# Kernel optimization log

Hardware: AMD Instinct MI355X
Metric: run time of the kernel (lower is better)

The kernel has to match this reference:

```python
import jax, jax.numpy as jnp
import numpy as np

DIM = 1024
WIN = 7
HEADS = 16
HEAD_DIM = DIM // HEADS
NT = WIN * WIN  # tokens per window = 49


def _relative_position_index():
    coords = np.stack(np.meshgrid(np.arange(WIN), np.arange(WIN), indexing='ij'))  # [2,W,W]
    cf = coords.reshape(2, -1)  # [2, NT]
    rel = cf[:, :, None] - cf[:, None, :]  # [2, NT, NT]
    rel = rel.transpose(1, 2, 0).copy()
    rel[:, :, 0] += WIN - 1
    rel[:, :, 1] += WIN - 1
    rel[:, :, 0] *= 2 * WIN - 1
    return jnp.asarray(rel.sum(-1), dtype=jnp.int32)  # [NT, NT]

REL_IDX = _relative_position_index()


def setup_inputs() -> dict:
    key = jax.random.key(0)
    ks = jax.random.split(key, 7)
    bsz_windows = 2048
    num_windows = 64
    x = jax.random.normal(ks[0], (bsz_windows, NT, DIM), dtype=jnp.float32)
    attn_mask = jax.random.normal(ks[1], (num_windows, NT, NT), dtype=jnp.float32)
    s = 0.02
    qkv_w = jax.random.normal(ks[2], (3 * DIM, DIM), dtype=jnp.float32) * s
    qkv_b = jnp.zeros((3 * DIM,), dtype=jnp.float32)
    proj_w = jax.random.normal(ks[3], (DIM, DIM), dtype=jnp.float32) * s
    proj_b = jnp.zeros((DIM,), dtype=jnp.float32)
    bias_table = jax.random.normal(ks[4], ((2 * WIN - 1) ** 2, HEADS), dtype=jnp.float32) * s
    return {"x": x, "attn_mask": attn_mask, "qkv_w": qkv_w, "qkv_b": qkv_b,
            "proj_w": proj_w, "proj_b": proj_b, "bias_table": bias_table}


def reference(x, attn_mask, qkv_w, qkv_b, proj_w, proj_b, bias_table):
    bw, nt, c = x.shape
    scale = HEAD_DIM ** -0.5
    qkv = x @ qkv_w.T + qkv_b  # [bw, nt, 3*dim]
    qkv = qkv.reshape(bw, nt, 3, HEADS, HEAD_DIM).transpose(2, 0, 3, 1, 4)
    q, k, v = qkv[0], qkv[1], qkv[2]  # each [bw, h, nt, hd]
    attn = jnp.einsum('bhqd,bhkd->bhqk', q * scale, k)  # [bw, h, nt, nt]
    rel_bias = bias_table[REL_IDX.reshape(-1)].reshape(nt, nt, HEADS).transpose(2, 0, 1)
    attn = attn + rel_bias[None]
    nw = attn_mask.shape[0]
    attn = attn.reshape(bw // nw, nw, HEADS, nt, nt) + attn_mask[None, :, None]
    attn = attn.reshape(bw, HEADS, nt, nt)
    attn = jax.nn.softmax(attn, axis=-1)
    out = jnp.einsum('bhqk,bhkd->bhqd', attn, v)
    out = out.transpose(0, 2, 1, 3).reshape(bw, nt, c)
    return out @ proj_w.T + proj_b
```

## Files before the change

### kernel.cpp

```cpp
#include <hip/hip_runtime.h>
#include <hip/hip_bf16.h>
#include <cstdint>
#include <cstddef>

#define HEADS 16
#define HD 64
#define NT 49
#define NTOK 3136
#define MROWS 100352
#define KDIM 1024

typedef __attribute__((ext_vector_type(4))) float f32x4;
typedef __attribute__((ext_vector_type(8))) short bf16x8;
typedef __attribute__((ext_vector_type(4))) unsigned short u16x4;

__device__ __forceinline__ unsigned short f2b(float f) {
  __hip_bfloat16 h = __float2bfloat16(f);
  return *reinterpret_cast<unsigned short*>(&h);
}
__device__ __forceinline__ float b2f(unsigned short u) {
  union { unsigned int i; float f; } c; c.i = ((unsigned int)u) << 16; return c.f;
}

__device__ __forceinline__ void gload16(const unsigned short* g, void* l) {
  __builtin_amdgcn_global_load_lds(
      (const __attribute__((address_space(1))) void*)g,
      (__attribute__((address_space(3))) void*)l, 16, 0, 0);
}

__device__ __forceinline__ void bar() {
  asm volatile("" ::: "memory");
  __builtin_amdgcn_s_barrier();
  asm volatile("" ::: "memory");
}

__global__ void cvt_f32_bf16(const float* __restrict__ s,
                             unsigned short* __restrict__ d, long n4) {
  long stride = (long)gridDim.x * blockDim.x;
  for (long i = blockIdx.x * (long)blockDim.x + threadIdx.x; i < n4; i += stride) {
    f32x4 v = reinterpret_cast<const f32x4*>(s)[i];
    u16x4 o;
    o.x = f2b(v.x); o.y = f2b(v.y); o.z = f2b(v.z); o.w = f2b(v.w);
    reinterpret_cast<u16x4*>(d)[i] = o;
  }
}

template<int EPI>
__global__ __launch_bounds__(512, 2)
void gemm_bt(const unsigned short* __restrict__ A,
             const unsigned short* __restrict__ B,
             const float* __restrict__ bias,
             void* __restrict__ Cout,
             const int nTilesN) {
  __shared__ __align__(16) unsigned short lds[2 * 2 * 256 * 64];

  const int nwg = gridDim.x;
  const int bid = blockIdx.x;
  const int cpx = nwg >> 3;
  const int swz = (bid & 7) * cpx + (bid >> 3);
  const int mt = swz / nTilesN;
  const int nt = swz - mt * nTilesN;
  const long mBase = (long)mt * 256;
  const int nBase = nt * 256;

  const int tid = threadIdx.x;
  const int lane = tid & 63;
  const int wid = tid >> 6;
  const int wr = wid >> 2;
  const int wc = wid & 3;
  const int lr = lane & 15;
  const int kg = lane >> 4;

  const int rbase = tid >> 3;
  const int c8 = (((tid & 7) ^ (rbase & 7)) << 3);
  const unsigned short* aSrc = A + (size_t)(mBase + rbase) * KDIM + c8;
  const unsigned short* bSrc = B + (size_t)(nBase + rbase) * KDIM + c8;
  char* ldsB = (char*)lds;

  f32x4 acc[8][4] = {};

  const int aRow = (wr * 128 + lr) * 64;
  const int bRow = (wc * 64 + lr) * 64;
  const int fOff0 = ((0 * 4 + kg) ^ (lr & 7)) << 3;
  const int fOff1 = ((1 * 4 + kg) ^ (lr & 7)) << 3;

#define STAGE(buf, kt) do {                                         \
    char* dA = ldsB + (buf) * 65536 + tid * 16;                     \
    const unsigned short* sA = aSrc + (kt) * 64;                    \
    const unsigned short* sB = bSrc + (kt) * 64;                    \
    _Pragma("unroll")                                               \
    for (int j = 0; j < 4; ++j)                                     \
      gload16(sA + (size_t)j * 64 * KDIM, dA + j * 8192);           \
    _Pragma("unroll")                                               \
    for (int j = 0; j < 4; ++j)                                     \
      gload16(sB + (size_t)j * 64 * KDIM, dA + 32768 + j * 8192);   \
  } while (0)

  STAGE(0, 0);
  STAGE(1, 1);
  asm volatile("s_waitcnt vmcnt(8)" ::: "memory");
  __builtin_amdgcn_sched_barrier(0);
  bar();

  for (int kt = 0; kt < KDIM / 64; ++kt) {
    const int cb = kt & 1;
    const unsigned short* As = lds + cb * 32768;
    const unsigned short* Bs = As + 16384;

    bf16x8 a0[4], a1[4], a2[4], a3[4], b0[4], b1[4];

#pragma unroll
    for (int j = 0; j < 4; ++j)
      a0[j] = *reinterpret_cast<const bf16x8*>(As + aRow + j * 1024 + fOff0);
#pragma unroll
    for (int n = 0; n < 4; ++n)
      b0[n] = *reinterpret_cast<const bf16x8*>(Bs + bRow + n * 1024 + fOff0);

    __builtin_amdgcn_s_setprio(1);
#pragma unroll
    for (int j = 0; j < 4; ++j)
      a1[j] = *reinterpret_cast<const bf16x8*>(As + aRow + (4 + j) * 1024 + fOff0);
#pragma unroll
    for (int j = 0; j < 4; ++j)
#pragma unroll
      for (int n = 0; n < 4; ++n)
        acc[j][n] = __builtin_amdgcn_mfma_f32_16x16x32_bf16(
            a0[j], b0[n], acc[j][n], 0, 0, 0);
    __builtin_amdgcn_s_setprio(0);
    bar();

    __builtin_amdgcn_s_setprio(1);
#pragma unroll
    for (int j = 0; j < 4; ++j)
      a2[j] = *reinterpret_cast<const bf16x8*>(As + aRow + j * 1024 + fOff1);
#pragma unroll
    for (int n = 0; n < 4; ++n)
      b1[n] = *reinterpret_cast<const bf16x8*>(Bs + bRow + n * 1024 + fOff1);
#pragma unroll
    for (int j = 0; j < 4; ++j)
#pragma unroll
      for (int n = 0; n < 4; ++n)
        acc[4 + j][n] = __builtin_amdgcn_mfma_f32_16x16x32_bf16(
            a1[j], b0[n], acc[4 + j][n], 0, 0, 0);
    __builtin_amdgcn_s_setprio(0);
    bar();

    __builtin_amdgcn_s_setprio(1);
#pragma unroll
    for (int j = 0; j < 4; ++j)
      a3[j] = *reinterpret_cast<const bf16x8*>(As + aRow + (4 + j) * 1024 + fOff1);
#pragma unroll
    for (int j = 0; j < 4; ++j)
#pragma unroll
      for (int n = 0; n < 4; ++n)
        acc[j][n] = __builtin_amdgcn_mfma_f32_16x16x32_bf16(
            a2[j], b1[n], acc[j][n], 0, 0, 0);
    __builtin_amdgcn_s_setprio(0);
    bar();

    __builtin_amdgcn_s_setprio(1);
#pragma unroll
    for (int j = 0; j < 4; ++j)
#pragma unroll
      for (int n = 0; n < 4; ++n)
        acc[4 + j][n] = __builtin_amdgcn_mfma_f32_16x16x32_bf16(
            a3[j], b1[n], acc[4 + j][n], 0, 0, 0);
    __builtin_amdgcn_s_setprio(0);
    bar();

    if (kt < KDIM / 64 - 2) {
      STAGE(cb, kt + 2);
      asm volatile("s_waitcnt vmcnt(8)" ::: "memory");
      __builtin_amdgcn_sched_barrier(0);
      bar();
    } else if (kt == KDIM / 64 - 2) {
      asm volatile("s_waitcnt vmcnt(0)" ::: "memory");
      __builtin_amdgcn_sched_barrier(0);
      bar();
    }
  }
#undef STAGE

  if (EPI == 0) {
    unsigned short* qkvbuf = (unsigned short*)Cout;
#pragma unroll
    for (int m = 0; m < 8; ++m) {
      const int row0 = wr * 128 + m * 16 + kg * 4;
#pragma unroll
      for (int n = 0; n < 4; ++n) {
        const int col = nBase + wc * 64 + n * 16 + lr;
        const int which = col >> 10;
        const int head = (col >> 6) & 15;
        const int d = col & 63;
        const float bv = bias[col];
#pragma unroll
        for (int r = 0; r < 4; ++r) {
          const int gm = (int)mBase + row0 + r;
          const int w = gm / NT;
          const int t = gm - w * NT;
          float v = acc[m][n][r] + bv;
          if (which == 0) v *= 0.125f;
          qkvbuf[(((size_t)w * 3 + which) * HEADS + head) * NTOK + t * HD + d] =
              f2b(v);
        }
      }
    }
  } else {
    float* out = (float*)Cout;
#pragma unroll
    for (int m = 0; m < 8; ++m) {
      const int row0 = wr * 128 + m * 16 + kg * 4;
#pragma unroll
      for (int n = 0; n < 4; ++n) {
        const int col = nBase + wc * 64 + n * 16 + lr;
        const float bv = bias[col];
#pragma unroll
        for (int r = 0; r < 4; ++r) {
          const int gm = (int)mBase + row0 + r;
          out[(size_t)gm * KDIM + col] = acc[m][n][r] + bv;
        }
      }
    }
  }
}

#define PSTR 72
#define VSTR 68

__global__ __launch_bounds__(64)
void attn_mfma(const unsigned short* __restrict__ qkv,
               const float* __restrict__ mask,
               const float* __restrict__ bias_table,
               unsigned short* __restrict__ aout) {
  const int blk = blockIdx.x;
  const int w = blk >> 4;
  const int h = blk & 15;
  const int lane = threadIdx.x;
  const int lr = lane & 15;
  const int kg = lane >> 4;

  __shared__ __align__(16) unsigned short Plds[64 * PSTR];
  __shared__ __align__(16) unsigned short Vlds[64 * VSTR];

  const unsigned short* qp = qkv + (((size_t)w * 3 + 0) * HEADS + h) * NTOK;
  const unsigned short* kp = qp + (size_t)HEADS * NTOK;
  const unsigned short* vp = qp + (size_t)2 * HEADS * NTOK;
  const float* mrow = mask + (size_t)(w & 63) * (NT * NT);

#pragma unroll
  for (int i = 0; i < 13; ++i) {
    const int idx = i * 64 + lane;
    if (idx < 784) {
      const int t = idx >> 4, c4 = (idx & 15) * 4;
      u16x4 vv = *reinterpret_cast<const u16x4*>(vp + t * HD + c4);
      *reinterpret_cast<u16x4*>(&Vlds[t * VSTR + c4]) = vv;
    }
  }
  {
    unsigned int* z = reinterpret_cast<unsigned int*>(&Vlds[49 * VSTR]);
#pragma unroll
    for (int i = 0; i < 8; ++i) {
      const int idx = i * 64 + lane;
      if (idx < 510) z[idx] = 0u;
    }
  }

  f32x4 acc[4][4];
  {
    int ibv[4], jbv[4];
#pragma unroll
    for (int n = 0; n < 4; ++n) {
      const int b = n * 16 + lr;
      ibv[n] = b / 7; jbv[n] = b % 7;
    }
#pragma unroll
    for (int m = 0; m < 4; ++m) {
#pragma unroll
      for (int r = 0; r < 4; ++r) {
        const int a = m * 16 + kg * 4 + r;
        const int ia = a / 7, ja = a % 7;
#pragma unroll
        for (int n = 0; n < 4; ++n) {
          const int b = n * 16 + lr;
          float v;
          if (b >= NT) v = -1e30f;
          else if (a >= NT) v = 0.f;
          else v = bias_table[((ia - ibv[n] + 6) * 13 + (ja - jbv[n] + 6)) * HEADS + h]
                 + mrow[a * NT + b];
          acc[m][n][r] = v;
        }
      }
    }
  }

#pragma unroll
  for (int ks = 0; ks < 2; ++ks) {
    bf16x8 af[4], bfr[4];
#pragma unroll
    for (int m = 0; m < 4; ++m) {
      int row = m * 16 + lr; if (row > 48) row = 48;
      af[m] = *reinterpret_cast<const bf16x8*>(qp + row * HD + ks * 32 + kg * 8);
    }
#pragma unroll
    for (int n = 0; n < 4; ++n) {
      int row = n * 16 + lr; if (row > 48) row = 48;
      bfr[n] = *reinterpret_cast<const bf16x8*>(kp + row * HD + ks * 32 + kg * 8);
    }
#pragma unroll
    for (int m = 0; m < 4; ++m)
#pragma unroll
      for (int n = 0; n < 4; ++n)
        acc[m][n] = __builtin_amdgcn_mfma_f32_16x16x32_bf16(
            af[m], bfr[n], acc[m][n], 0, 0, 0);
  }

#pragma unroll
  for (int m = 0; m < 4; ++m) {
#pragma unroll
    for (int r = 0; r < 4; ++r) {
      float mx = fmaxf(fmaxf(acc[m][0][r], acc[m][1][r]),
                       fmaxf(acc[m][2][r], acc[m][3][r]));
      mx = fmaxf(mx, __shfl_xor(mx, 1));
      mx = fmaxf(mx, __shfl_xor(mx, 2));
      mx = fmaxf(mx, __shfl_xor(mx, 4));
      mx = fmaxf(mx, __shfl_xor(mx, 8));
      float s = 0.f;
#pragma unroll
      for (int n = 0; n < 4; ++n) {
        const float e = __expf(acc[m][n][r] - mx);
        acc[m][n][r] = e;
        s += e;
      }
      s += __shfl_xor(s, 1);
      s += __shfl_xor(s, 2);
      s += __shfl_xor(s, 4);
      s += __shfl_xor(s, 8);
      const float si = 1.0f / s;
#pragma unroll
      for (int n = 0; n < 4; ++n) acc[m][n][r] *= si;
    }
  }
  __syncthreads();

#pragma unroll
  for (int m = 0; m < 4; ++m)
#pragma unroll
    for (int n = 0; n < 4; ++n)
#pragma unroll
      for (int r = 0; r < 4; ++r)
        Plds[(m * 16 + kg * 4 + r) * PSTR + n * 16 + lr] = f2b(acc[m][n][r]);
  __syncthreads();

  f32x4 acc2[4][4] = {};
#pragma unroll
  for (int ks = 0; ks < 2; ++ks) {
    bf16x8 pf[4], vf[4];
#pragma unroll
    for (int m = 0; m < 4; ++m)
      pf[m] = *reinterpret_cast<const bf16x8*>(
          &Plds[(m * 16 + lr) * PSTR + ks * 32 + kg * 8]);
#pragma unroll
    for (int n = 0; n < 4; ++n) {
      union { bf16x8 v; unsigned short u[8]; } vu;
#pragma unroll
      for (int j = 0; j < 8; ++j)
        vu.u[j] = Vlds[(ks * 32 + kg * 8 + j) * VSTR + n * 16 + lr];
      vf[n] = vu.v;
    }
#pragma unroll
    for (int m = 0; m < 4; ++m)
#pragma unroll
      for (int n = 0; n < 4; ++n)
        acc2[m][n] = __builtin_amdgcn_mfma_f32_16x16x32_bf16(
            pf[m], vf[n], acc2[m][n], 0, 0, 0);
  }

#pragma unroll
  for (int m = 0; m < 4; ++m) {
#pragma unroll
    for (int r = 0; r < 4; ++r) {
      const int a = m * 16 + kg * 4 + r;
      if (a >= NT) continue;
#pragma unroll
      for (int n = 0; n < 4; ++n) {
        const int d = n * 16 + lr;
        aout[((size_t)(w * NT + a)) * KDIM + h * HD + d] = f2b(acc2[m][n][r]);
      }
    }
  }
}

extern "C" void kernel_launch(void* const* d_in, const int* in_sizes, int n_in,
                              void* d_out, int out_size, void* d_ws, size_t ws_size,
                              hipStream_t stream) {
  const float* x          = (const float*)d_in[0];
  const float* attn_mask  = (const float*)d_in[1];
  const float* qkv_w      = (const float*)d_in[2];
  const float* qkv_b      = (const float*)d_in[3];
  const float* proj_w     = (const float*)d_in[4];
  const float* proj_b     = (const float*)d_in[5];
  const float* bias_table = (const float*)d_in[6];
  float* out = (float*)d_out;

  char* ws = (char*)d_ws;
  const size_t xbf_bytes = (size_t)MROWS * KDIM * 2;
  unsigned short* xbf      = (unsigned short*)ws;
  unsigned short* qkvw_bf  = (unsigned short*)(ws + xbf_bytes);
  unsigned short* projw_bf = qkvw_bf + 3072 * 1024;
  unsigned short* qkvbuf   = (unsigned short*)(ws + xbf_bytes + 8388608);
  unsigned short* aout     = xbf;

  cvt_f32_bf16<<<8192, 256, 0, stream>>>(x, xbf, (long)MROWS * KDIM / 4);
  cvt_f32_bf16<<<3072, 256, 0, stream>>>(qkv_w, qkvw_bf, (long)3072 * 1024 / 4);
  cvt_f32_bf16<<<1024, 256, 0, stream>>>(proj_w, projw_bf, (long)1024 * 1024 / 4);

  gemm_bt<0><<<392 * 12, 512, 0, stream>>>(xbf, qkvw_bf, qkv_b, (void*)qkvbuf, 12);

  attn_mfma<<<2048 * HEADS, 64, 0, stream>>>(qkvbuf, attn_mask, bias_table, aout);

  gemm_bt<1><<<392 * 4, 512, 0, stream>>>(aout, projw_bf, proj_b, (void*)out, 4);
}
```

Baseline: 1.600 ms.

## Split window-head attention across four waves per block

The attention kernel now launches 256 threads per block and gives each wave one 16-row query tile, instead of one wave handling all four tiles. V staging into shared memory is spread across all threads, and a barrier is added before compute. Each wave holds far fewer accumulators, which lowers register pressure and raises parallelism per window-head. In exchange, every wave reloads the K fragments and there is more block-level synchronisation.

```diff
diff --git a/kernel.cpp b/kernel.cpp
--- a/kernel.cpp
+++ b/kernel.cpp
@@ -227,7 +227,7 @@
 #define PSTR 72
 #define VSTR 68
 
-__global__ __launch_bounds__(64)
+__global__ __launch_bounds__(256, 8)
 void attn_mfma(const unsigned short* __restrict__ qkv,
                const float* __restrict__ mask,
                const float* __restrict__ bias_table,
@@ -235,7 +235,9 @@
   const int blk = blockIdx.x;
   const int w = blk >> 4;
   const int h = blk & 15;
-  const int lane = threadIdx.x;
+  const int tid = threadIdx.x;
+  const int lane = tid & 63;
+  const int wv = tid >> 6;
   const int lr = lane & 15;
   const int kg = lane >> 4;
 
@@ -248,8 +250,8 @@
   const float* mrow = mask + (size_t)(w & 63) * (NT * NT);
 
 #pragma unroll
-  for (int i = 0; i < 13; ++i) {
-    const int idx = i * 64 + lane;
+  for (int i = 0; i < 4; ++i) {
+    const int idx = i * 256 + tid;
     if (idx < 784) {
       const int t = idx >> 4, c4 = (idx & 15) * 4;
       u16x4 vv = *reinterpret_cast<const u16x4*>(vp + t * HD + c4);
@@ -259,133 +261,100 @@
   {
     unsigned int* z = reinterpret_cast<unsigned int*>(&Vlds[49 * VSTR]);
 #pragma unroll
-    for (int i = 0; i < 8; ++i) {
-      const int idx = i * 64 + lane;
+    for (int i = 0; i < 2; ++i) {
+      const int idx = i * 256 + tid;
       if (idx < 510) z[idx] = 0u;
     }
   }
-
-  f32x4 acc[4][4];
+  __syncthreads();
+
+  const int a0 = wv * 16 + kg * 4;
+  f32x4 acc[4];
   {
-    int ibv[4], jbv[4];
-#pragma unroll
-    for (int n = 0; n < 4; ++n) {
-      const int b = n * 16 + lr;
-      ibv[n] = b / 7; jbv[n] = b % 7;
-    }
-#pragma unroll
-    for (int m = 0; m < 4; ++m) {
-#pragma unroll
-      for (int r = 0; r < 4; ++r) {
-        const int a = m * 16 + kg * 4 + r;
-        const int ia = a / 7, ja = a % 7;
-#pragma unroll
-        for (int n = 0; n < 4; ++n) {
-          const int b = n * 16 + lr;
-          float v;
-          if (b >= NT) v = -1e30f;
-          else if (a >= NT) v = 0.f;
-          else v = bias_table[((ia - ibv[n] + 6) * 13 + (ja - jbv[n] + 6)) * HEADS + h]
-                 + mrow[a * NT + b];
-          acc[m][n][r] = v;
-        }
+#pragma unroll
+    for (int r = 0; r < 4; ++r) {
+      const int a = a0 + r;
+      const int ia = a / 7, ja = a % 7;
+#pragma unroll
+      for (int n = 0; n < 4; ++n) {
+        const int b = n * 16 + lr;
+        const int ib = b / 7, jb = b % 7;
+        float v;
+        if (b >= NT) v = -1e30f;
+        else if (a >= NT) v = 0.f;
+        else v = bias_table[((ia - ib + 6) * 13 + (ja - jb + 6)) * HEADS + h]
+               + mrow[a * NT + b];
+        acc[n][r] = v;
       }
     }
   }
 
+  int qrow = wv * 16 + lr; if (qrow > 48) qrow = 48;
 #pragma unroll
   for (int ks = 0; ks < 2; ++ks) {
-    bf16x8 af[4], bfr[4];
-#pragma unroll
-    for (int m = 0; m < 4; ++m) {
-      int row = m * 16 + lr; if (row > 48) row = 48;
-      af[m] = *reinterpret_cast<const bf16x8*>(qp + row * HD + ks * 32 + kg * 8);
-    }
+    bf16x8 af = *reinterpret_cast<const bf16x8*>(qp + qrow * HD + ks * 32 + kg * 8);
 #pragma unroll
     for (int n = 0; n < 4; ++n) {
       int row = n * 16 + lr; if (row > 48) row = 48;
-      bfr[n] = *reinterpret_cast<const bf16x8*>(kp + row * HD + ks * 32 + kg * 8);
-    }
-#pragma unroll
-    for (int m = 0; m < 4; ++m)
-#pragma unroll
-      for (int n = 0; n < 4; ++n)
-        acc[m][n] = __builtin_amdgcn_mfma_f32_16x16x32_bf16(
-            af[m], bfr[n], acc[m][n], 0, 0, 0);
-  }
-
-#pragma unroll
-  for (int m = 0; m < 4; ++m) {
-#pragma unroll
-    for (int r = 0; r < 4; ++r) {
-      float mx = fmaxf(fmaxf(acc[m][0][r], acc[m][1][r]),
-                       fmaxf(acc[m][2][r], acc[m][3][r]));
-      mx = fmaxf(mx, __shfl_xor(mx, 1));
-      mx = fmaxf(mx, __shfl_xor(mx, 2));
-      mx = fmaxf(mx, __shfl_xor(mx, 4));
-      mx = fmaxf(mx, __shfl_xor(mx, 8));
-      float s = 0.f;
-#pragma unroll
-      for (int n = 0; n < 4; ++n) {
-        const float e = __expf(acc[m][n][r] - mx);
-        acc[m][n][r] = e;
-        s += e;
-      }
-      s += __shfl_xor(s, 1);
-      s += __shfl_xor(s, 2);
-      s += __shfl_xor(s, 4);
-      s += __shfl_xor(s, 8);
-      const float si = 1.0f / s;
-#pragma unroll
-      for (int n = 0; n < 4; ++n) acc[m][n][r] *= si;
-    }
-  }
-  __syncthreads();
-
-#pragma unroll
-  for (int m = 0; m < 4; ++m)
-#pragma unroll
-    for (int n = 0; n < 4; ++n)
-#pragma unroll
-      for (int r = 0; r < 4; ++r)
-        Plds[(m * 16 + kg * 4 + r) * PSTR + n * 16 + lr] = f2b(acc[m][n][r]);
-  __syncthreads();
-
-  f32x4 acc2[4][4] = {};
+      bf16x8 bfr = *reinterpret_cast<const bf16x8*>(kp + row * HD + ks * 32 + kg * 8);
+      acc[n] = __builtin_amdgcn_mfma_f32_16x16x32_bf16(af, bfr, acc[n], 0, 0, 0);
+    }
+  }
+
+#pragma unroll
+  for (int r = 0; r < 4; ++r) {
+    float mx = fmaxf(fmaxf(acc[0][r], acc[1][r]),
+                     fmaxf(acc[2][r], acc[3][r]));
+    mx = fmaxf(mx, __shfl_xor(mx, 1));
+    mx = fmaxf(mx, __shfl_xor(mx, 2));
+    mx = fmaxf(mx, __shfl_xor(mx, 4));
+    mx = fmaxf(mx, __shfl_xor(mx, 8));
+    float s = 0.f;
+#pragma unroll
+    for (int n = 0; n < 4; ++n) {
+      const float e = __expf(acc[n][r] - mx);
+      acc[n][r] = e;
+      s += e;
+    }
+    s += __shfl_xor(s, 1);
+    s += __shfl_xor(s, 2);
+    s += __shfl_xor(s, 4);
+    s += __shfl_xor(s, 8);
+    const float si = 1.0f / s;
+#pragma unroll
+    for (int n = 0; n < 4; ++n) acc[n][r] *= si;
+  }
+
+#pragma unroll
+  for (int n = 0; n < 4; ++n)
+#pragma unroll
+    for (int r = 0; r < 4; ++r)
+      Plds[(a0 + r) * PSTR + n * 16 + lr] = f2b(acc[n][r]);
+
+  f32x4 acc2[4] = {};
+  const int prow = wv * 16 + lr;
 #pragma unroll
   for (int ks = 0; ks < 2; ++ks) {
-    bf16x8 pf[4], vf[4];
-#pragma unroll
-    for (int m = 0; m < 4; ++m)
-      pf[m] = *reinterpret_cast<const bf16x8*>(
-          &Plds[(m * 16 + lr) * PSTR + ks * 32 + kg * 8]);
+    bf16x8 pf = *reinterpret_cast<const bf16x8*>(
+        &Plds[prow * PSTR + ks * 32 + kg * 8]);
 #pragma unroll
     for (int n = 0; n < 4; ++n) {
       union { bf16x8 v; unsigned short u[8]; } vu;
 #pragma unroll
       for (int j = 0; j < 8; ++j)
         vu.u[j] = Vlds[(ks * 32 + kg * 8 + j) * VSTR + n * 16 + lr];
-      vf[n] = vu.v;
-    }
-#pragma unroll
-    for (int m = 0; m < 4; ++m)
-#pragma unroll
-      for (int n = 0; n < 4; ++n)
-        acc2[m][n] = __builtin_amdgcn_mfma_f32_16x16x32_bf16(
-            pf[m], vf[n], acc2[m][n], 0, 0, 0);
-  }
-
-#pragma unroll
-  for (int m = 0; m < 4; ++m) {
-#pragma unroll
-    for (int r = 0; r < 4; ++r) {
-      const int a = m * 16 + kg * 4 + r;
-      if (a >= NT) continue;
-#pragma unroll
-      for (int n = 0; n < 4; ++n) {
-        const int d = n * 16 + lr;
-        aout[((size_t)(w * NT + a)) * KDIM + h * HD + d] = f2b(acc2[m][n][r]);
-      }
+      acc2[n] = __builtin_amdgcn_mfma_f32_16x16x32_bf16(pf, vu.v, acc2[n], 0, 0, 0);
+    }
+  }
+
+#pragma unroll
+  for (int r = 0; r < 4; ++r) {
+    const int a = a0 + r;
+    if (a >= NT) continue;
+#pragma unroll
+    for (int n = 0; n < 4; ++n) {
+      const int d = n * 16 + lr;
+      aout[((size_t)(w * NT + a)) * KDIM + h * HD + d] = f2b(acc2[n][r]);
     }
   }
 }
@@ -416,7 +385,7 @@
 
   gemm_bt<0><<<392 * 12, 512, 0, stream>>>(xbf, qkvw_bf, qkv_b, (void*)qkvbuf, 12);
 
-  attn_mfma<<<2048 * HEADS, 64, 0, stream>>>(qkvbuf, attn_mask, bias_table, aout);
+  attn_mfma<<<2048 * HEADS, 256, 0, stream>>>(qkvbuf, attn_mask, bias_table, aout);
 
   gemm_bt<1><<<392 * 4, 512, 0, stream>>>(aout, projw_bf, proj_b, (void*)out, 4);
 }
```

After: 1.509 ms. 1.06x faster.
